# Kernel tuning notes

Measured on AMD Instinct MI355X. Metric: run time of the kernel, lower is better.

Reference implementation:

```python
import jax, jax.numpy as jnp
import numpy as np
from jax import lax

EPS = 1e-7  # keras K.epsilon()
DN = ('NHWC', 'HWIO', 'NHWC')


def _box_avg(z, k):
    """Depthwise k x k box filter with SAME padding, scaled by 1/(k*k*C).
    Matches tf.nn.depthwise_conv2d with a ones/(k*k*C) kernel, implemented
    separably (two 1D convs) for efficiency."""
    C = z.shape[-1]
    scale = 1.0 / (k * k * C)  # note: keras code divides by full kernel size incl. C
    kh = jnp.ones((k, 1, 1, C), z.dtype)
    kw = jnp.ones((1, k, 1, C), z.dtype)
    z = lax.conv_general_dilated(z, kh, (1, 1), 'SAME',
                                 dimension_numbers=DN, feature_group_count=C)
    z = lax.conv_general_dilated(z, kw, (1, 1), 'SAME',
                                 dimension_numbers=DN, feature_group_count=C)
    return z * scale


def setup_inputs() -> dict:
    key = jax.random.key(0)
    x = jax.random.normal(key, (8, 1024, 1024, 2), dtype=jnp.float32)
    return {"x": x, "filter_size": 61}


def reference(x, filter_size):
    k = int(filter_size)
    # norm_method == 'std':
    out = x - _box_avg(x, k)                       # local mean-subtract
    c1 = _box_avg(out, k)
    c2 = _box_avg(out * out, k)
    std = jnp.sqrt(c2 - c1 * c1) + EPS             # local window std
    return out / std
```

## Files before the change

kernel.cpp:

```cpp
#include <hip/hip_runtime.h>
#include <math.h>

#define NB 8
#define HH 1024
#define WW 1024
#define RAD 30
#define KS 61
#define ROWSZ 2048
#define IMGSZ (HH * ROWSZ)
#define STR2 1024
#define STR4 512
#define NCOL4 (NB * STR4)
#define VSEGH 16
#define VNSEG (HH / VSEGH)
#define EPSV 1e-7f
#define SCALEV (1.0f / (float)(KS * KS * 2))
#define PDW (WW + WW / 8)
#define PD(i) ((i) + ((i) >> 3))

__device__ __forceinline__ unsigned bf16_rn(float f) {
    unsigned u = __float_as_uint(f);
    return (u + 0x7FFFu + ((u >> 16) & 1u)) >> 16;
}
__device__ __forceinline__ unsigned pk2(float a, float b) {
    return bf16_rn(a) | (bf16_rn(b) << 16);
}
__device__ __forceinline__ float2 up2(unsigned u) {
    return make_float2(__uint_as_float(u << 16),
                       __uint_as_float(u & 0xFFFF0000u));
}
__device__ __forceinline__ float2 f2add(float2 a, float2 b) {
    return make_float2(a.x + b.x, a.y + b.y);
}
__device__ __forceinline__ float2 f2sub(float2 a, float2 b) {
    return make_float2(a.x - b.x, a.y - b.y);
}
__device__ __forceinline__ float sqrt_f(float x) { return __builtin_amdgcn_sqrtf(x); }
__device__ __forceinline__ float rcp_f(float x)  { return __builtin_amdgcn_rcpf(x); }

__global__ __launch_bounds__(256) void vbox_kernel(const float* __restrict__ in,
                                                   unsigned* __restrict__ out) {
    int tid = blockIdx.x * 256 + threadIdx.x;
    int col = tid & (NCOL4 - 1);
    int seg = tid >> 12;
    int n = col >> 9;
    int c = col & (STR4 - 1);
    const float4* ip = (const float4*)(in + (size_t)n * IMGSZ) + c;
    uint2* op = (uint2*)(out + (size_t)n * (IMGSZ / 2)) + c;
    int h0 = seg * VSEGH;
    float4 S = make_float4(0.f, 0.f, 0.f, 0.f);
    int lo = h0 - RAD; if (lo < 0) lo = 0;
    int hiend = h0 + RAD; if (hiend > HH) hiend = HH;
    int h = lo;
    for (; h + 8 <= hiend; h += 8) {
        float4 W[8];
        #pragma unroll
        for (int i = 0; i < 8; ++i) W[i] = ip[(h + i) * STR4];
        __builtin_amdgcn_sched_barrier(0);
        #pragma unroll
        for (int i = 0; i < 8; ++i) {
            S.x += W[i].x; S.y += W[i].y; S.z += W[i].z; S.w += W[i].w;
        }
    }
    for (; h < hiend; ++h) {
        float4 w = ip[h * STR4];
        S.x += w.x; S.y += w.y; S.z += w.z; S.w += w.w;
    }

    if (h0 >= RAD && h0 + VSEGH + RAD <= HH) {
        const float4* lp = ip + (h0 + RAD) * STR4;
        const float4* tp = ip + (h0 - RAD) * STR4;
        uint2* opp = op + (size_t)h0 * STR4;
        float4 LA[8], TA[8], LB[8], TB[8];
#define VB_LOAD(Lx, Tx, r) { \
        _Pragma("unroll") for (int i = 0; i < 8; ++i) Lx[i] = lp[((r) + i) * STR4]; \
        _Pragma("unroll") for (int i = 0; i < 8; ++i) Tx[i] = tp[((r) + i) * STR4]; \
        __builtin_amdgcn_sched_barrier(0); }
#define VB_CONS(Lx, Tx, r) { \
        _Pragma("unroll") for (int i = 0; i < 8; ++i) { \
            S.x += Lx[i].x; S.y += Lx[i].y; S.z += Lx[i].z; S.w += Lx[i].w; \
            opp[((r) + i) * STR4] = make_uint2(pk2(S.x, S.y), pk2(S.z, S.w)); \
            S.x -= Tx[i].x; S.y -= Tx[i].y; S.z -= Tx[i].z; S.w -= Tx[i].w; } }
        VB_LOAD(LA, TA, 0)
        VB_LOAD(LB, TB, 8)
        VB_CONS(LA, TA, 0)
        VB_CONS(LB, TB, 8)
#undef VB_LOAD
#undef VB_CONS
    } else {
        const float4 Z = make_float4(0.f, 0.f, 0.f, 0.f);
        for (int ho = h0; ho < h0 + VSEGH; ho += 4) {
            float4 a[4], b[4];
            #pragma unroll
            for (int i = 0; i < 4; ++i) {
                int ha = ho + i + RAD;
                a[i] = (ha < HH) ? ip[ha * STR4] : Z;
            }
            #pragma unroll
            for (int i = 0; i < 4; ++i) {
                int hb = ho + i - RAD;
                b[i] = (hb >= 0) ? ip[hb * STR4] : Z;
            }
            #pragma unroll
            for (int i = 0; i < 4; ++i) {
                S.x += a[i].x; S.y += a[i].y; S.z += a[i].z; S.w += a[i].w;
                op[(size_t)(ho + i) * STR4] = make_uint2(pk2(S.x, S.y), pk2(S.z, S.w));
                S.x -= b[i].x; S.y -= b[i].y; S.z -= b[i].z; S.w -= b[i].w;
            }
        }
    }
}

__device__ inline float wave_incl_scan(float v) {
    int lane = threadIdx.x & 63;
    #pragma unroll
    for (int d = 1; d < 64; d <<= 1) {
        float o = __shfl_up(v, d, 64);
        if (lane >= d) v += o;
    }
    return v;
}

__global__ __launch_bounds__(256) void hmid_kernel(const unsigned* __restrict__ vsum,
                                                   const float* __restrict__ x,
                                                   float* __restrict__ out,
                                                   uint2* __restrict__ hig) {
    __shared__ float ch[2][PDW];
    __shared__ float s4[4][PDW];
    __shared__ float wtot[4];
    int t = threadIdx.x;
    size_t g = (size_t)blockIdx.x * ROWSZ;
    const uint4* vrow = (const uint4*)(vsum + (size_t)blockIdx.x * STR2);
    uint4 u = vrow[t];
    {
        float2 p0 = up2(u.x), p1 = up2(u.y), p2 = up2(u.z), p3 = up2(u.w);
        int w = 4 * t;
        ch[0][PD(w + 0)] = p0.x; ch[1][PD(w + 0)] = p0.y;
        ch[0][PD(w + 1)] = p1.x; ch[1][PD(w + 1)] = p1.y;
        ch[0][PD(w + 2)] = p2.x; ch[1][PD(w + 2)] = p2.y;
        ch[0][PD(w + 3)] = p3.x; ch[1][PD(w + 3)] = p3.y;
    }
    __syncthreads();
    {
        int c = t >> 7, j = t & 127, base = j * 8;
        float v[8]; float run = 0.f;
        #pragma unroll
        for (int i = 0; i < 8; ++i) { run += ch[c][PD(base + i)]; v[i] = run; }
        float incl = wave_incl_scan(run);
        int wid = t >> 6;
        if ((t & 63) == 63) wtot[wid] = incl;
        __syncthreads();
        float off = incl - run;
        if (wid & 1) off += wtot[wid - 1];
        #pragma unroll
        for (int i = 0; i < 8; ++i) ch[c][PD(base + i)] = off + v[i];
    }
    __syncthreads();
    const float4* xrow = (const float4*)(x + g);
    float4* orow = (float4*)(out + g);
    #pragma unroll
    for (int i = 0; i < 2; ++i) {
        int jj = t + 256 * i;
        int w0 = 2 * jj, w1 = 2 * jj + 1;
        int hi0 = w0 + RAD; if (hi0 > WW - 1) hi0 = WW - 1;
        int hi1 = w1 + RAD; if (hi1 > WW - 1) hi1 = WW - 1;
        int lo0 = w0 - RAD - 1, lo1 = w1 - RAD - 1;
        float s00 = ch[0][PD(hi0)], s10 = ch[1][PD(hi0)];
        if (lo0 >= 0) { s00 -= ch[0][PD(lo0)]; s10 -= ch[1][PD(lo0)]; }
        float s01 = ch[0][PD(hi1)], s11 = ch[1][PD(hi1)];
        if (lo1 >= 0) { s01 -= ch[0][PD(lo1)]; s11 -= ch[1][PD(lo1)]; }
        float4 xv = xrow[jj];
        float4 o;
        o.x = xv.x - SCALEV * s00; o.y = xv.y - SCALEV * s10;
        o.z = xv.z - SCALEV * s01; o.w = xv.w - SCALEV * s11;
        orow[jj] = o;
        s4[0][PD(w0)] = o.x;       s4[1][PD(w0)] = o.y;
        s4[0][PD(w1)] = o.z;       s4[1][PD(w1)] = o.w;
        s4[2][PD(w0)] = o.x * o.x; s4[3][PD(w0)] = o.y * o.y;
        s4[2][PD(w1)] = o.z * o.z; s4[3][PD(w1)] = o.w * o.w;
    }
    __syncthreads();
    {
        int a = t >> 6, j = t & 63, base = j * 16;
        float v[16]; float run = 0.f;
        #pragma unroll
        for (int i = 0; i < 16; ++i) { run += s4[a][PD(base + i)]; v[i] = run; }
        float incl = wave_incl_scan(run);
        float off = incl - run;
        #pragma unroll
        for (int i = 0; i < 16; ++i) s4[a][PD(base + i)] = off + v[i];
    }
    __syncthreads();
    uint4* hirow = (uint4*)(hig + (size_t)blockIdx.x * STR2);
    #pragma unroll
    for (int i = 0; i < 2; ++i) {
        int jj = t + 256 * i;
        int w0 = 2 * jj, w1 = 2 * jj + 1;
        int hi0 = w0 + RAD; if (hi0 > WW - 1) hi0 = WW - 1;
        int hi1 = w1 + RAD; if (hi1 > WW - 1) hi1 = WW - 1;
        int lo0 = w0 - RAD - 1, lo1 = w1 - RAD - 1;
        float a00 = s4[0][PD(hi0)], a10 = s4[1][PD(hi0)];
        float q00 = s4[2][PD(hi0)], q10 = s4[3][PD(hi0)];
        if (lo0 >= 0) {
            a00 -= s4[0][PD(lo0)]; a10 -= s4[1][PD(lo0)];
            q00 -= s4[2][PD(lo0)]; q10 -= s4[3][PD(lo0)];
        }
        float a01 = s4[0][PD(hi1)], a11 = s4[1][PD(hi1)];
        float q01 = s4[2][PD(hi1)], q11 = s4[3][PD(hi1)];
        if (lo1 >= 0) {
            a01 -= s4[0][PD(lo1)]; a11 -= s4[1][PD(lo1)];
            q01 -= s4[2][PD(lo1)]; q11 -= s4[3][PD(lo1)];
        }
        hirow[jj] = make_uint4(pk2(a00, a10), pk2(q00, q10),
                               pk2(a01, a11), pk2(q01, q11));
    }
}

__global__ __launch_bounds__(256) void vfinal_kernel(const uint2* __restrict__ hi,
                                                     float* __restrict__ io) {
    int tid = blockIdx.x * 256 + threadIdx.x;
    int col = tid & (NCOL4 - 1);
    int seg = tid >> 12;
    int n = col >> 9;
    int c = col & (STR4 - 1);
    const uint4* pp = (const uint4*)(hi + (size_t)n * (size_t)HH * STR2) + c;
    float4* op = (float4*)(io + (size_t)n * IMGSZ) + c;
    int h0 = seg * VSEGH;
    float2 S1a = make_float2(0.f, 0.f), S2a = make_float2(0.f, 0.f);
    float2 S1b = make_float2(0.f, 0.f), S2b = make_float2(0.f, 0.f);
    int lo = h0 - RAD; if (lo < 0) lo = 0;
    int hiend = h0 + RAD; if (hiend > HH) hiend = HH;
    int h = lo;
    for (; h + 8 <= hiend; h += 8) {
        uint4 A[8];
        #pragma unroll
        for (int i = 0; i < 8; ++i) A[i] = pp[(h + i) * STR4];
        __builtin_amdgcn_sched_barrier(0);
        #pragma unroll
        for (int i = 0; i < 8; ++i) {
            S1a = f2add(S1a, up2(A[i].x)); S2a = f2add(S2a, up2(A[i].y));
            S1b = f2add(S1b, up2(A[i].z)); S2b = f2add(S2b, up2(A[i].w));
        }
    }
    for (; h < hiend; ++h) {
        uint4 v = pp[h * STR4];
        S1a = f2add(S1a, up2(v.x)); S2a = f2add(S2a, up2(v.y));
        S1b = f2add(S1b, up2(v.z)); S2b = f2add(S2b, up2(v.w));
    }

#define VF_ROW(Ai, Oi, Ti, ro) { \
    S1a = f2add(S1a, up2((Ai).x)); S2a = f2add(S2a, up2((Ai).y)); \
    S1b = f2add(S1b, up2((Ai).z)); S2b = f2add(S2b, up2((Ai).w)); \
    float4 yv; \
    yv.x = (Oi).x * rcp_f(sqrt_f(fmaxf(SCALEV * S2a.x - (SCALEV * S1a.x) * (SCALEV * S1a.x), 0.f)) + EPSV); \
    yv.y = (Oi).y * rcp_f(sqrt_f(fmaxf(SCALEV * S2a.y - (SCALEV * S1a.y) * (SCALEV * S1a.y), 0.f)) + EPSV); \
    yv.z = (Oi).z * rcp_f(sqrt_f(fmaxf(SCALEV * S2b.x - (SCALEV * S1b.x) * (SCALEV * S1b.x), 0.f)) + EPSV); \
    yv.w = (Oi).w * rcp_f(sqrt_f(fmaxf(SCALEV * S2b.y - (SCALEV * S1b.y) * (SCALEV * S1b.y), 0.f)) + EPSV); \
    oq[(ro) * STR4] = yv; \
    S1a = f2sub(S1a, up2((Ti).x)); S2a = f2sub(S2a, up2((Ti).y)); \
    S1b = f2sub(S1b, up2((Ti).z)); S2b = f2sub(S2b, up2((Ti).w)); \
}

    if (h0 >= RAD && h0 + VSEGH + RAD <= HH) {
        const uint4* lp = pp + (h0 + RAD) * STR4;
        const uint4* tp = pp + (h0 - RAD) * STR4;
        float4* oq = op + (size_t)h0 * STR4;
        uint4 LA[8], TA[8], LB[8], TB[8];
        float4 OA[8], OB[8];
#define VF_LOAD(Lx, Tx, Ox, r) { \
        _Pragma("unroll") for (int i = 0; i < 8; ++i) Lx[i] = lp[((r) + i) * STR4]; \
        _Pragma("unroll") for (int i = 0; i < 8; ++i) Tx[i] = tp[((r) + i) * STR4]; \
        _Pragma("unroll") for (int i = 0; i < 8; ++i) Ox[i] = oq[((r) + i) * STR4]; \
        __builtin_amdgcn_sched_barrier(0); }
#define VF_CONS(Lx, Tx, Ox, r) { \
        _Pragma("unroll") for (int i = 0; i < 8; ++i) VF_ROW(Lx[i], Ox[i], Tx[i], (r) + i) }
        VF_LOAD(LA, TA, OA, 0)
        VF_LOAD(LB, TB, OB, 8)
        VF_CONS(LA, TA, OA, 0)
        VF_CONS(LB, TB, OB, 8)
#undef VF_LOAD
#undef VF_CONS
    } else {
        const uint4 Z4 = make_uint4(0u, 0u, 0u, 0u);
        float4* oq = op;
        for (int ho = h0; ho < h0 + VSEGH; ho += 4) {
            uint4 a[4], b[4];
            float4 O[4];
            #pragma unroll
            for (int i = 0; i < 4; ++i) {
                int ha = ho + i + RAD;
                a[i] = (ha < HH) ? pp[ha * STR4] : Z4;
            }
            #pragma unroll
            for (int i = 0; i < 4; ++i) {
                int hb = ho + i - RAD;
                b[i] = (hb >= 0) ? pp[hb * STR4] : Z4;
            }
            #pragma unroll
            for (int i = 0; i < 4; ++i) O[i] = op[(size_t)(ho + i) * STR4];
            #pragma unroll
            for (int i = 0; i < 4; ++i) {
                VF_ROW(a[i], O[i], b[i], (size_t)(ho + i))
            }
        }
        (void)oq;
    }
#undef VF_ROW
}

extern "C" void kernel_launch(void* const* d_in, const int* in_sizes, int n_in,
                              void* d_out, int out_size, void* d_ws, size_t ws_size,
                              hipStream_t stream) {
    const float* x = (const float*)d_in[0];
    float* out = (float*)d_out;
    unsigned* V1 = (unsigned*)d_ws;
    uint2* HI = (uint2*)(V1 + (size_t)NB * IMGSZ / 2);

    int vgrid = (NCOL4 * VNSEG) / 256;
    vbox_kernel<<<vgrid, 256, 0, stream>>>(x, V1);
    hmid_kernel<<<NB * HH, 256, 0, stream>>>(V1, x, out, HI);
    vfinal_kernel<<<vgrid, 256, 0, stream>>>(HI, out);
}
```

Before: 225.3 us.

## Store mean-subtracted intermediate as fp16 and double vertical segment height

The mean-subtracted intermediate is now written by hmid as packed fp16 into the workspace, reusing the first-pass buffer, instead of as fp32 into the output. vfinal reads it back from there, which halves that round trip's bytes. The vertical segment height goes from 16 to 32 rows, with the software-pipelined load/consume sequence extended to match. This amortizes the 60-row prefix warm-up each segment pays over twice as many outputs, at the cost of fewer threads and some fp16 rounding of the intermediate.

```diff
diff --git a/kernel.cpp b/kernel.cpp
--- a/kernel.cpp
+++ b/kernel.cpp
@@ -1,4 +1,5 @@
 #include <hip/hip_runtime.h>
+#include <hip/hip_fp16.h>
 #include <math.h>
 
 #define NB 8
@@ -11,7 +12,7 @@
 #define STR2 1024
 #define STR4 512
 #define NCOL4 (NB * STR4)
-#define VSEGH 16
+#define VSEGH 32
 #define VNSEG (HH / VSEGH)
 #define EPSV 1e-7f
 #define SCALEV (1.0f / (float)(KS * KS * 2))
@@ -28,6 +29,14 @@
 __device__ __forceinline__ float2 up2(unsigned u) {
     return make_float2(__uint_as_float(u << 16),
                        __uint_as_float(u & 0xFFFF0000u));
+}
+__device__ __forceinline__ unsigned pkh(float a, float b) {
+    __half2 h = __floats2half2_rn(a, b);
+    return *reinterpret_cast<unsigned*>(&h);
+}
+__device__ __forceinline__ float2 uph(unsigned u) {
+    __half2 h = *reinterpret_cast<__half2*>(&u);
+    return __half22float2(h);
 }
 __device__ __forceinline__ float2 f2add(float2 a, float2 b) {
     return make_float2(a.x + b.x, a.y + b.y);
@@ -84,7 +93,11 @@
         VB_LOAD(LA, TA, 0)
         VB_LOAD(LB, TB, 8)
         VB_CONS(LA, TA, 0)
+        VB_LOAD(LA, TA, 16)
         VB_CONS(LB, TB, 8)
+        VB_LOAD(LB, TB, 24)
+        VB_CONS(LA, TA, 16)
+        VB_CONS(LB, TB, 24)
 #undef VB_LOAD
 #undef VB_CONS
     } else {
@@ -123,7 +136,7 @@
 
 __global__ __launch_bounds__(256) void hmid_kernel(const unsigned* __restrict__ vsum,
                                                    const float* __restrict__ x,
-                                                   float* __restrict__ out,
+                                                   unsigned* __restrict__ oh,
                                                    uint2* __restrict__ hig) {
     __shared__ float ch[2][PDW];
     __shared__ float s4[4][PDW];
@@ -157,7 +170,7 @@
     }
     __syncthreads();
     const float4* xrow = (const float4*)(x + g);
-    float4* orow = (float4*)(out + g);
+    uint2* ohrow = (uint2*)(oh + (size_t)blockIdx.x * STR2);
     #pragma unroll
     for (int i = 0; i < 2; ++i) {
         int jj = t + 256 * i;
@@ -173,7 +186,7 @@
         float4 o;
         o.x = xv.x - SCALEV * s00; o.y = xv.y - SCALEV * s10;
         o.z = xv.z - SCALEV * s01; o.w = xv.w - SCALEV * s11;
-        orow[jj] = o;
+        ohrow[jj] = make_uint2(pkh(o.x, o.y), pkh(o.z, o.w));
         s4[0][PD(w0)] = o.x;       s4[1][PD(w0)] = o.y;
         s4[0][PD(w1)] = o.z;       s4[1][PD(w1)] = o.w;
         s4[2][PD(w0)] = o.x * o.x; s4[3][PD(w0)] = o.y * o.y;
@@ -217,14 +230,16 @@
 }
 
 __global__ __launch_bounds__(256) void vfinal_kernel(const uint2* __restrict__ hi,
-                                                     float* __restrict__ io) {
+                                                     const unsigned* __restrict__ oh,
+                                                     float* __restrict__ fout) {
     int tid = blockIdx.x * 256 + threadIdx.x;
     int col = tid & (NCOL4 - 1);
     int seg = tid >> 12;
     int n = col >> 9;
     int c = col & (STR4 - 1);
     const uint4* pp = (const uint4*)(hi + (size_t)n * (size_t)HH * STR2) + c;
-    float4* op = (float4*)(io + (size_t)n * IMGSZ) + c;
+    const uint2* po = (const uint2*)(oh + (size_t)n * (IMGSZ / 2)) + c;
+    float4* fo = (float4*)(fout + (size_t)n * IMGSZ) + c;
     int h0 = seg * VSEGH;
     float2 S1a = make_float2(0.f, 0.f), S2a = make_float2(0.f, 0.f);
     float2 S1b = make_float2(0.f, 0.f), S2b = make_float2(0.f, 0.f);
@@ -251,11 +266,12 @@
 #define VF_ROW(Ai, Oi, Ti, ro) { \
     S1a = f2add(S1a, up2((Ai).x)); S2a = f2add(S2a, up2((Ai).y)); \
     S1b = f2add(S1b, up2((Ai).z)); S2b = f2add(S2b, up2((Ai).w)); \
+    float2 oA = uph((Oi).x), oB = uph((Oi).y); \
     float4 yv; \
-    yv.x = (Oi).x * rcp_f(sqrt_f(fmaxf(SCALEV * S2a.x - (SCALEV * S1a.x) * (SCALEV * S1a.x), 0.f)) + EPSV); \
-    yv.y = (Oi).y * rcp_f(sqrt_f(fmaxf(SCALEV * S2a.y - (SCALEV * S1a.y) * (SCALEV * S1a.y), 0.f)) + EPSV); \
-    yv.z = (Oi).z * rcp_f(sqrt_f(fmaxf(SCALEV * S2b.x - (SCALEV * S1b.x) * (SCALEV * S1b.x), 0.f)) + EPSV); \
-    yv.w = (Oi).w * rcp_f(sqrt_f(fmaxf(SCALEV * S2b.y - (SCALEV * S1b.y) * (SCALEV * S1b.y), 0.f)) + EPSV); \
+    yv.x = oA.x * rcp_f(sqrt_f(fmaxf(SCALEV * S2a.x - (SCALEV * S1a.x) * (SCALEV * S1a.x), 0.f)) + EPSV); \
+    yv.y = oA.y * rcp_f(sqrt_f(fmaxf(SCALEV * S2a.y - (SCALEV * S1a.y) * (SCALEV * S1a.y), 0.f)) + EPSV); \
+    yv.z = oB.x * rcp_f(sqrt_f(fmaxf(SCALEV * S2b.x - (SCALEV * S1b.x) * (SCALEV * S1b.x), 0.f)) + EPSV); \
+    yv.w = oB.y * rcp_f(sqrt_f(fmaxf(SCALEV * S2b.y - (SCALEV * S1b.y) * (SCALEV * S1b.y), 0.f)) + EPSV); \
     oq[(ro) * STR4] = yv; \
     S1a = f2sub(S1a, up2((Ti).x)); S2a = f2sub(S2a, up2((Ti).y)); \
     S1b = f2sub(S1b, up2((Ti).z)); S2b = f2sub(S2b, up2((Ti).w)); \
@@ -264,28 +280,33 @@
     if (h0 >= RAD && h0 + VSEGH + RAD <= HH) {
         const uint4* lp = pp + (h0 + RAD) * STR4;
         const uint4* tp = pp + (h0 - RAD) * STR4;
-        float4* oq = op + (size_t)h0 * STR4;
+        const uint2* orp = po + (size_t)h0 * STR4;
+        float4* oq = fo + (size_t)h0 * STR4;
         uint4 LA[8], TA[8], LB[8], TB[8];
-        float4 OA[8], OB[8];
+        uint2 OA[8], OB[8];
 #define VF_LOAD(Lx, Tx, Ox, r) { \
         _Pragma("unroll") for (int i = 0; i < 8; ++i) Lx[i] = lp[((r) + i) * STR4]; \
         _Pragma("unroll") for (int i = 0; i < 8; ++i) Tx[i] = tp[((r) + i) * STR4]; \
-        _Pragma("unroll") for (int i = 0; i < 8; ++i) Ox[i] = oq[((r) + i) * STR4]; \
+        _Pragma("unroll") for (int i = 0; i < 8; ++i) Ox[i] = orp[((r) + i) * STR4]; \
         __builtin_amdgcn_sched_barrier(0); }
 #define VF_CONS(Lx, Tx, Ox, r) { \
         _Pragma("unroll") for (int i = 0; i < 8; ++i) VF_ROW(Lx[i], Ox[i], Tx[i], (r) + i) }
         VF_LOAD(LA, TA, OA, 0)
         VF_LOAD(LB, TB, OB, 8)
         VF_CONS(LA, TA, OA, 0)
+        VF_LOAD(LA, TA, OA, 16)
         VF_CONS(LB, TB, OB, 8)
+        VF_LOAD(LB, TB, OB, 24)
+        VF_CONS(LA, TA, OA, 16)
+        VF_CONS(LB, TB, OB, 24)
 #undef VF_LOAD
 #undef VF_CONS
     } else {
         const uint4 Z4 = make_uint4(0u, 0u, 0u, 0u);
-        float4* oq = op;
+        float4* oq = fo;
         for (int ho = h0; ho < h0 + VSEGH; ho += 4) {
             uint4 a[4], b[4];
-            float4 O[4];
+            uint2 O[4];
             #pragma unroll
             for (int i = 0; i < 4; ++i) {
                 int ha = ho + i + RAD;
@@ -297,7 +318,7 @@
                 b[i] = (hb >= 0) ? pp[hb * STR4] : Z4;
             }
             #pragma unroll
-            for (int i = 0; i < 4; ++i) O[i] = op[(size_t)(ho + i) * STR4];
+            for (int i = 0; i < 4; ++i) O[i] = po[(size_t)(ho + i) * STR4];
             #pragma unroll
             for (int i = 0; i < 4; ++i) {
                 VF_ROW(a[i], O[i], b[i], (size_t)(ho + i))
@@ -314,10 +335,11 @@
     const float* x = (const float*)d_in[0];
     float* out = (float*)d_out;
     unsigned* V1 = (unsigned*)d_ws;
+    unsigned* OH = V1;
     uint2* HI = (uint2*)(V1 + (size_t)NB * IMGSZ / 2);
 
     int vgrid = (NCOL4 * VNSEG) / 256;
     vbox_kernel<<<vgrid, 256, 0, stream>>>(x, V1);
-    hmid_kernel<<<NB * HH, 256, 0, stream>>>(V1, x, out, HI);
-    vfinal_kernel<<<vgrid, 256, 0, stream>>>(HI, out);
-}
+    hmid_kernel<<<NB * HH, 256, 0, stream>>>(V1, x, OH, HI);
+    vfinal_kernel<<<vgrid, 256, 0, stream>>>(HI, OH, out);
+}
```

New measurement: 208.6 us. 7.4% less time.
